# Performance work log

Measured on AMD Instinct MI355X. Metric: run time of the kernel, lower is better.

Reference implementation:

```python
import jax, jax.numpy as jnp
import numpy as np


def setup_inputs() -> dict:
    key = jax.random.key(0)
    k1, k2, k3, k4 = jax.random.split(key, 4)
    n, m = 4096, 1024  # n video frames, 1024-d features
    scale = 0.02
    return {
        "x": jax.random.normal(k1, (n, m), dtype=jnp.float32),
        "WQ": jax.random.normal(k2, (m, m), dtype=jnp.float32) * scale,  # torch Linear weight [out,in]
        "WK": jax.random.normal(k3, (m, m), dtype=jnp.float32) * scale,
        "WV": jax.random.normal(k4, (m, m), dtype=jnp.float32) * scale,
    }


def _quaternion_logits(q, k):
    """Hamilton-product attention logits: 4 tensors of shape [Lq, Lk]."""
    qr, qx, qy, qz = jnp.split(q, 4, axis=-1)
    kr, kx, ky, kz = jnp.split(k, 4, axis=-1)
    dot = lambda a, b: jnp.einsum('qd,kd->qk', a, b)
    r = dot(qr, kr) - dot(qx, kx) - dot(qy, ky) - dot(qz, kz)
    i = dot(qr, kx) + dot(qx, kr) + dot(qy, kz) - dot(qz, ky)
    j = dot(qr, ky) - dot(qx, kz) + dot(qy, kr) + dot(qz, kx)
    kk = dot(qr, kz) + dot(qx, ky) - dot(qy, kx) + dot(qz, kr)
    return [r, i, j, kk]


def reference(x, WQ, WK, WV):
    # QKV projections (torch Linear, no bias): y = x @ W.T
    Q = x @ WQ.T
    K = x @ WK.T
    V = x @ WV.T
    v_vals = jnp.split(V, 4, axis=-1)  # 4 chunks of depth d/4 (tensor2tensor quaternion attn)
    logits = _quaternion_logits(Q, K)
    outs = []
    w = None
    for l, v in zip(logits, v_vals):
        w = jax.nn.softmax(l, axis=-1)  # per-component softmax over keys
        outs.append(w @ v)
    y = jnp.concatenate(outs, axis=-1)  # [n, d]
    # original returns the attention weights from the last component (loop-leaked var)
    return y, w
```

## Files before the change

kernel.cpp:

```cpp
#include <hip/hip_runtime.h>
#include <cmath>

typedef __attribute__((ext_vector_type(8))) short short8;
typedef __attribute__((ext_vector_type(8))) _Float16 half8;
typedef __attribute__((ext_vector_type(4))) float f32x4;
typedef unsigned short u16;

__device__ __forceinline__ u16 f2h(float f) {
    _Float16 h = (_Float16)f;
    return __builtin_bit_cast(u16, h);
}
__device__ __forceinline__ float h2f(u16 b) {
    return (float)__builtin_bit_cast(_Float16, b);
}

#define GLD16(g, l)                                                              \
    __builtin_amdgcn_global_load_lds(                                            \
        (const __attribute__((address_space(1))) unsigned int*)(g),              \
        (__attribute__((address_space(3))) unsigned int*)(l), 16, 0, 0)

#define MFMA_F16(a, b, c)                                                        \
    __builtin_amdgcn_mfma_f32_16x16x32_f16(                                      \
        __builtin_bit_cast(half8, (a)), __builtin_bit_cast(half8, (b)), (c), 0, 0, 0)
#define SBAR() asm volatile("s_barrier" ::: "memory")

__global__ __launch_bounds__(256) void to_h(const float* __restrict__ in,
                                            u16* __restrict__ out) {
    int idx = blockIdx.x * 256 + threadIdx.x;
    float4 v = reinterpret_cast<const float4*>(in)[idx];
    ushort4 h;
    h.x = f2h(v.x); h.y = f2h(v.y); h.z = f2h(v.z); h.w = f2h(v.w);
    reinterpret_cast<ushort4*>(out)[idx] = h;
}

__global__ __launch_bounds__(512, 2) void logits8(
    const u16* __restrict__ A, const u16* __restrict__ B, const u16* __restrict__ Bneg,
    u16* __restrict__ Ch, float* __restrict__ pm, float* __restrict__ ps,
    int perm_packed, int sign_packed)
{
    constexpr int NT = 16;
    __shared__ u16 L[2][2][256 * 64];
    const int tid = threadIdx.x;
    const int l = tid & 63, w = tid >> 6;
    const int wr = w >> 2, wc = w & 3;
    const int lr = l & 15, lh = l >> 4;
    const int bid = (int)blockIdx.x;
    const int swz = (bid & 7) * 32 + (bid >> 3);
    const int row0 = (swz >> 4) * 256, col0 = (swz & 15) * 256;
    const int srow = l >> 3;
    const int scol = ((l & 7) ^ (l >> 3)) * 8;

    f32x4 acc[8][4] = {};

    auto stage = [&](int t) {
        int kA = t * 64;
        int ch = kA >> 8;
        int p = (perm_packed >> (2 * ch)) & 3;
        const u16* Bsrc = ((sign_packed >> ch) & 1) ? Bneg : B;
        int kB = (p << 8) + (kA & 255);
        int bf = t & 1;
        #pragma unroll
        for (int i = 0; i < 4; ++i) {
            int r0 = w * 32 + i * 8;
            GLD16(&A[(size_t)(row0 + r0 + srow) * 1024 + kA + scol], &L[bf][0][r0 * 64]);
        }
        #pragma unroll
        for (int i = 0; i < 4; ++i) {
            int r0 = w * 32 + i * 8;
            GLD16(&Bsrc[(size_t)(col0 + r0 + srow) * 1024 + kB + scol], &L[bf][1][r0 * 64]);
        }
    };
    auto readA = [&](int bf, int m, int kh) -> short8 {
        int row = wr * 128 + m * 16 + lr;
        int c = ((kh * 4 + lh) ^ (lr & 7)) * 8;
        return *reinterpret_cast<const short8*>(&L[bf][0][row * 64 + c]);
    };
    auto readB = [&](int bf, int n, int kh) -> short8 {
        int row = wc * 64 + n * 16 + lr;
        int c = ((kh * 4 + lh) ^ (lr & 7)) * 8;
        return *reinterpret_cast<const short8*>(&L[bf][1][row * 64 + c]);
    };

    stage(0);
    stage(1);
    asm volatile("s_waitcnt vmcnt(8)" ::: "memory");
    SBAR();

    #pragma unroll 2
    for (int t = 0; t < NT; ++t) {
        const int bf = t & 1;
        short8 am[4][2], bn[4][2];
        #pragma unroll
        for (int m = 0; m < 4; ++m) { am[m][0] = readA(bf, m, 0); am[m][1] = readA(bf, m, 1); }
        #pragma unroll
        for (int n = 0; n < 2; ++n) { bn[n][0] = readB(bf, n, 0); bn[n][1] = readB(bf, n, 1); }
        SBAR();
        __builtin_amdgcn_s_setprio(1);
        #pragma unroll
        for (int m = 0; m < 4; ++m)
            #pragma unroll
            for (int n = 0; n < 2; ++n) {
                acc[m][n] = MFMA_F16(am[m][0], bn[n][0], acc[m][n]);
                acc[m][n] = MFMA_F16(am[m][1], bn[n][1], acc[m][n]);
            }
        __builtin_amdgcn_s_setprio(0);
        SBAR();
        #pragma unroll
        for (int n = 2; n < 4; ++n) { bn[n][0] = readB(bf, n, 0); bn[n][1] = readB(bf, n, 1); }
        SBAR();
        __builtin_amdgcn_s_setprio(1);
        #pragma unroll
        for (int m = 0; m < 4; ++m)
            #pragma unroll
            for (int n = 2; n < 4; ++n) {
                acc[m][n] = MFMA_F16(am[m][0], bn[n][0], acc[m][n]);
                acc[m][n] = MFMA_F16(am[m][1], bn[n][1], acc[m][n]);
            }
        __builtin_amdgcn_s_setprio(0);
        SBAR();
        #pragma unroll
        for (int m = 0; m < 4; ++m) { am[m][0] = readA(bf, 4 + m, 0); am[m][1] = readA(bf, 4 + m, 1); }
        SBAR();
        __builtin_amdgcn_s_setprio(1);
        #pragma unroll
        for (int m = 0; m < 4; ++m)
            #pragma unroll
            for (int n = 2; n < 4; ++n) {
                acc[4 + m][n] = MFMA_F16(am[m][0], bn[n][0], acc[4 + m][n]);
                acc[4 + m][n] = MFMA_F16(am[m][1], bn[n][1], acc[4 + m][n]);
            }
        __builtin_amdgcn_s_setprio(0);
        SBAR();
        if (t + 2 < NT) stage(t + 2);
        SBAR();
        __builtin_amdgcn_s_setprio(1);
        #pragma unroll
        for (int m = 0; m < 4; ++m)
            #pragma unroll
            for (int n = 0; n < 2; ++n) {
                acc[4 + m][n] = MFMA_F16(am[m][0], bn[n][0], acc[4 + m][n]);
                acc[4 + m][n] = MFMA_F16(am[m][1], bn[n][1], acc[4 + m][n]);
            }
        __builtin_amdgcn_s_setprio(0);
        if (t + 2 < NT) { asm volatile("s_waitcnt vmcnt(8)" ::: "memory"); }
        else           { asm volatile("s_waitcnt vmcnt(0)" ::: "memory"); }
        SBAR();
    }

    const int tcol = (col0 >> 6) + wc;
    #pragma unroll
    for (int m = 0; m < 8; ++m) {
        #pragma unroll
        for (int j = 0; j < 4; ++j) {
            int row = row0 + wr * 128 + m * 16 + lh * 4 + j;
            float v = fmaxf(fmaxf(acc[m][0][j], acc[m][1][j]),
                            fmaxf(acc[m][2][j], acc[m][3][j]));
            #pragma unroll
            for (int off = 1; off < 16; off <<= 1) v = fmaxf(v, __shfl_xor(v, off, 16));
            float s = expf(acc[m][0][j] - v) + expf(acc[m][1][j] - v)
                    + expf(acc[m][2][j] - v) + expf(acc[m][3][j] - v);
            #pragma unroll
            for (int off = 1; off < 16; off <<= 1) s += __shfl_xor(s, off, 16);
            if (lr == 0) {
                pm[(size_t)row * 64 + tcol] = v;
                ps[(size_t)row * 64 + tcol] = s;
            }
            #pragma unroll
            for (int n = 0; n < 4; ++n) {
                int gc = col0 + wc * 64 + n * 16 + lr;
                Ch[(size_t)row * 4096 + gc] = f2h(acc[m][n][j] - v);
            }
        }
    }
}

__global__ __launch_bounds__(512, 2) void qkv8(
    const u16* __restrict__ A, const u16* __restrict__ B,
    u16* __restrict__ Qh, u16* __restrict__ Kh, u16* __restrict__ Khn,
    u16* __restrict__ Vt)
{
    constexpr int NT = 16;
    __shared__ u16 L[2][2][256 * 64];
    const int tid = threadIdx.x;
    const int l = tid & 63, w = tid >> 6;
    const int wr = w >> 2, wc = w & 3;
    const int lr = l & 15, lh = l >> 4;
    const int bid = (int)blockIdx.x;
    const int wgid = (bid & 7) * 24 + (bid >> 3);
    const int row0 = (wgid / 12) * 256, col0 = (wgid % 12) * 256;
    const int srow = l >> 3;
    const int scol = ((l & 7) ^ (l >> 3)) * 8;

    f32x4 acc[8][4] = {};

    auto stage = [&](int t) {
        int k0 = t * 64;
        int bf = t & 1;
        #pragma unroll
        for (int i = 0; i < 4; ++i) {
            int r0 = w * 32 + i * 8;
            GLD16(&A[(size_t)(row0 + r0 + srow) * 1024 + k0 + scol], &L[bf][0][r0 * 64]);
        }
        #pragma unroll
        for (int i = 0; i < 4; ++i) {
            int r0 = w * 32 + i * 8;
            GLD16(&B[(size_t)(col0 + r0 + srow) * 1024 + k0 + scol], &L[bf][1][r0 * 64]);
        }
    };
    auto readA = [&](int bf, int m, int kh) -> short8 {
        int row = wr * 128 + m * 16 + lr;
        int c = ((kh * 4 + lh) ^ (lr & 7)) * 8;
        return *reinterpret_cast<const short8*>(&L[bf][0][row * 64 + c]);
    };
    auto readB = [&](int bf, int n, int kh) -> short8 {
        int row = wc * 64 + n * 16 + lr;
        int c = ((kh * 4 + lh) ^ (lr & 7)) * 8;
        return *reinterpret_cast<const short8*>(&L[bf][1][row * 64 + c]);
    };

    stage(0);
    stage(1);
    asm volatile("s_waitcnt vmcnt(8)" ::: "memory");
    SBAR();

    #pragma unroll 2
    for (int t = 0; t < NT; ++t) {
        const int bf = t & 1;
        short8 am[4][2], bn[4][2];
        #pragma unroll
        for (int m = 0; m < 4; ++m) { am[m][0] = readA(bf, m, 0); am[m][1] = readA(bf, m, 1); }
        #pragma unroll
        for (int n = 0; n < 2; ++n) { bn[n][0] = readB(bf, n, 0); bn[n][1] = readB(bf, n, 1); }
        SBAR();
        __builtin_amdgcn_s_setprio(1);
        #pragma unroll
        for (int m = 0; m < 4; ++m)
            #pragma unroll
            for (int n = 0; n < 2; ++n) {
                acc[m][n] = MFMA_F16(am[m][0], bn[n][0], acc[m][n]);
                acc[m][n] = MFMA_F16(am[m][1], bn[n][1], acc[m][n]);
            }
        __builtin_amdgcn_s_setprio(0);
        SBAR();
        #pragma unroll
        for (int n = 2; n < 4; ++n) { bn[n][0] = readB(bf, n, 0); bn[n][1] = readB(bf, n, 1); }
        SBAR();
        __builtin_amdgcn_s_setprio(1);
        #pragma unroll
        for (int m = 0; m < 4; ++m)
            #pragma unroll
            for (int n = 2; n < 4; ++n) {
                acc[m][n] = MFMA_F16(am[m][0], bn[n][0], acc[m][n]);
                acc[m][n] = MFMA_F16(am[m][1], bn[n][1], acc[m][n]);
            }
        __builtin_amdgcn_s_setprio(0);
        SBAR();
        #pragma unroll
        for (int m = 0; m < 4; ++m) { am[m][0] = readA(bf, 4 + m, 0); am[m][1] = readA(bf, 4 + m, 1); }
        SBAR();
        __builtin_amdgcn_s_setprio(1);
        #pragma unroll
        for (int m = 0; m < 4; ++m)
            #pragma unroll
            for (int n = 2; n < 4; ++n) {
                acc[4 + m][n] = MFMA_F16(am[m][0], bn[n][0], acc[4 + m][n]);
                acc[4 + m][n] = MFMA_F16(am[m][1], bn[n][1], acc[4 + m][n]);
            }
        __builtin_amdgcn_s_setprio(0);
        SBAR();
        if (t + 2 < NT) stage(t + 2);
        SBAR();
        __builtin_amdgcn_s_setprio(1);
        #pragma unroll
        for (int m = 0; m < 4; ++m)
            #pragma unroll
            for (int n = 0; n < 2; ++n) {
                acc[4 + m][n] = MFMA_F16(am[m][0], bn[n][0], acc[4 + m][n]);
                acc[4 + m][n] = MFMA_F16(am[m][1], bn[n][1], acc[4 + m][n]);
            }
        __builtin_amdgcn_s_setprio(0);
        if (t + 2 < NT) { asm volatile("s_waitcnt vmcnt(8)" ::: "memory"); }
        else           { asm volatile("s_waitcnt vmcnt(0)" ::: "memory"); }
        SBAR();
    }

    const int mode = col0 >> 10;
    #pragma unroll
    for (int m = 0; m < 8; ++m)
        #pragma unroll
        for (int n = 0; n < 4; ++n) {
            int gr = row0 + wr * 128 + m * 16 + lh * 4;
            int gc = col0 + wc * 64 + n * 16 + lr;
            int gcl = gc & 1023;
            f32x4 v = acc[m][n];
            if (mode == 0) {
                #pragma unroll
                for (int j = 0; j < 4; ++j)
                    Qh[(size_t)(gr + j) * 1024 + gcl] = f2h(v[j]);
            } else if (mode == 1) {
                #pragma unroll
                for (int j = 0; j < 4; ++j) {
                    u16 h = f2h(v[j]);
                    size_t o = (size_t)(gr + j) * 1024 + gcl;
                    Kh[o] = h; Khn[o] = h ^ 0x8000;
                }
            } else {
                ushort4 o;
                o.x = f2h(v[0]); o.y = f2h(v[1]); o.z = f2h(v[2]); o.w = f2h(v[3]);
                *reinterpret_cast<ushort4*>(&Vt[(size_t)gcl * 4096 + gr]) = o;
            }
        }
}

template<bool WRITE_W>
__global__ __launch_bounds__(256) void pv_fused(
    const u16* __restrict__ Lh, float* __restrict__ Wout,
    const u16* __restrict__ Vt, const float* __restrict__ pm,
    const float* __restrict__ ps, u16* __restrict__ ypart, int c256)
{
    __shared__ u16 As[64 * 64];
    __shared__ u16 Bs[256 * 64];
    __shared__ float Red[64][4];
    __shared__ float Ms[64], Is[64];
    const int tid = threadIdx.x;
    const int l = tid & 63, w = tid >> 6;
    const int lr = l & 15, lh = l >> 4;
    const int kc = blockIdx.x;
    const int row0 = blockIdx.y * 64;
    const int kbase = kc * 512;
    const int srow = l >> 3, scol = ((l & 7) ^ (l >> 3)) * 8;

    {
        int row = tid & 63, part = tid >> 6;
        const float* pmr = &pm[(size_t)(row0 + row) * 64 + part * 16];
        const float* psr = &ps[(size_t)(row0 + row) * 64 + part * 16];
        float M = -INFINITY;
        #pragma unroll
        for (int i = 0; i < 16; ++i) M = fmaxf(M, pmr[i]);
        Red[row][part] = M;
        __syncthreads();
        float Mg = fmaxf(fmaxf(Red[row][0], Red[row][1]),
                         fmaxf(Red[row][2], Red[row][3]));
        float S = 0.f;
        #pragma unroll
        for (int i = 0; i < 16; ++i) S += psr[i] * expf(pmr[i] - Mg);
        __syncthreads();
        Red[row][part] = S;
        __syncthreads();
        if (tid < 64) {
            float Sg = Red[tid][0] + Red[tid][1] + Red[tid][2] + Red[tid][3];
            Ms[tid] = Mg;
            Is[tid] = 1.0f / Sg;
        }
        __syncthreads();
    }

    float Mr[4], Ir[4];
    #pragma unroll
    for (int i = 0; i < 4; ++i) { int r = (tid >> 4) + i * 16; Mr[i] = Ms[r]; Ir[i] = Is[r]; }

    f32x4 acc[4][4] = {};

    for (int kt = 0; kt < 8; ++kt) {
        const int tcol = kc * 8 + kt;
        __syncthreads();
        #pragma unroll
        for (int i = 0; i < 4; ++i) {
            int idx = tid + i * 256;
            int r = idx >> 4, s4 = idx & 15;
            float coff = pm[(size_t)(row0 + r) * 64 + tcol] - Mr[i];
            size_t ga = (size_t)(row0 + r) * 4096 + kbase + kt * 64 + s4 * 4;
            ushort4 dv = *reinterpret_cast<const ushort4*>(&Lh[ga]);
            float e0 = expf(h2f(dv.x) + coff) * Ir[i];
            float e1 = expf(h2f(dv.y) + coff) * Ir[i];
            float e2 = expf(h2f(dv.z) + coff) * Ir[i];
            float e3 = expf(h2f(dv.w) + coff) * Ir[i];
            if (WRITE_W)
                *reinterpret_cast<float4*>(&Wout[ga]) = make_float4(e0, e1, e2, e3);
            ushort4 h;
            h.x = f2h(e0); h.y = f2h(e1); h.z = f2h(e2); h.w = f2h(e3);
            int dst = ((s4 >> 1) ^ (r & 7)) * 8 + (s4 & 1) * 4;
            *reinterpret_cast<ushort4*>(&As[r * 64 + dst]) = h;
        }
        #pragma unroll
        for (int i = 0; i < 8; ++i) {
            int r0 = w * 64 + i * 8;
            GLD16(&Vt[(size_t)(c256 + r0 + srow) * 4096 + kbase + kt * 64 + scol],
                  &Bs[r0 * 64]);
        }
        __syncthreads();
        #pragma unroll
        for (int kh = 0; kh < 2; ++kh) {
            short8 af[4], bfv[4];
            #pragma unroll
            for (int m = 0; m < 4; ++m)
                af[m] = *reinterpret_cast<const short8*>(
                    &As[(m * 16 + lr) * 64 + ((kh * 4 + lh) ^ (lr & 7)) * 8]);
            #pragma unroll
            for (int n = 0; n < 4; ++n)
                bfv[n] = *reinterpret_cast<const short8*>(
                    &Bs[(w * 64 + n * 16 + lr) * 64 + ((kh * 4 + lh) ^ (lr & 7)) * 8]);
            #pragma unroll
            for (int m = 0; m < 4; ++m)
                #pragma unroll
                for (int n = 0; n < 4; ++n)
                    acc[m][n] = MFMA_F16(af[m], bfv[n], acc[m][n]);
        }
    }

    #pragma unroll
    for (int m = 0; m < 4; ++m)
        #pragma unroll
        for (int n = 0; n < 4; ++n) {
            int rr = m * 16 + lh * 4;
            int col = w * 64 + n * 16 + lr;
            #pragma unroll
            for (int j = 0; j < 4; ++j)
                ypart[((size_t)kc * 4096 + row0 + rr + j) * 256 + col] = f2h(acc[m][n][j]);
        }
}

__global__ __launch_bounds__(256) void reduce_y(const u16* __restrict__ ypart,
                                                float* __restrict__ y, int c256)
{
    int idx = blockIdx.x * 256 + threadIdx.x;
    int r = idx >> 6, c4 = (idx & 63) * 4;
    float s0 = 0.f, s1 = 0.f, s2 = 0.f, s3 = 0.f;
    #pragma unroll
    for (int kc = 0; kc < 8; ++kc) {
        ushort4 p = *reinterpret_cast<const ushort4*>(
            &ypart[((size_t)kc * 4096 + r) * 256 + c4]);
        s0 += h2f(p.x); s1 += h2f(p.y); s2 += h2f(p.z); s3 += h2f(p.w);
    }
    *reinterpret_cast<float4*>(&y[(size_t)r * 1024 + c256 + c4]) =
        make_float4(s0, s1, s2, s3);
}

extern "C" void kernel_launch(void* const* d_in, const int* in_sizes, int n_in,
                              void* d_out, int out_size, void* d_ws, size_t ws_size,
                              hipStream_t stream)
{
    const int n = 4096, d = 1024;
    const float* x  = (const float*)d_in[0];
    const float* WQ = (const float*)d_in[1];
    const float* WK = (const float*)d_in[2];
    const float* WV = (const float*)d_in[3];

    float* y = (float*)d_out;
    float* wout = y + (size_t)n * d;

    u16* Lh   = (u16*)d_ws;
    u16* xh   = Lh;
    u16* Wh   = Lh + (size_t)n * 1024;
    u16* Qh   = Lh + (size_t)n * 4096;
    u16* Kh   = Qh  + (size_t)n * 1024;
    u16* Khn  = Kh  + (size_t)n * 1024;
    u16* Vt   = Khn + (size_t)n * 1024;
    u16* ypart = Vt + (size_t)d * 4096;
    float* pm = (float*)(ypart + (size_t)8 * n * 256);
    float* ps = pm + (size_t)n * 64;

    to_h<<<n * d / 1024, 256, 0, stream>>>(x, xh);
    to_h<<<d * d / 1024, 256, 0, stream>>>(WQ, Wh);
    to_h<<<d * d / 1024, 256, 0, stream>>>(WK, Wh + (size_t)d * 1024);
    to_h<<<d * d / 1024, 256, 0, stream>>>(WV, Wh + (size_t)2 * d * 1024);

    qkv8<<<192, 512, 0, stream>>>(xh, Wh, Qh, Kh, Khn, Vt);

    const int permv[4] = {0xE4, 0xB1, 0x4E, 0x1B};
    const int signv[4] = {0x0E, 0x08, 0x02, 0x04};

    for (int c = 0; c < 4; ++c) {
        logits8<<<256, 512, 0, stream>>>(Qh, Kh, Khn, Lh, pm, ps, permv[c], signv[c]);
        if (c == 3)
            pv_fused<true><<<dim3(8, 64), 256, 0, stream>>>(Lh, wout, Vt, pm, ps, ypart, c * 256);
        else
            pv_fused<false><<<dim3(8, 64), 256, 0, stream>>>(Lh, wout, Vt, pm, ps, ypart, c * 256);
        reduce_y<<<1024, 256, 0, stream>>>(ypart, y, c * 256);
    }
}
```

Before: 374.3 us.

## Fuse conversions, negate A in registers, store exp in logits, atomic-add partial outputs

Folds the four fp16 conversion launches into one kernel. Drops the negated-K copy and instead flips sign bits on the A fragments in registers. The logits kernel now stores exp(l - local max) instead of raw offsets, so the PV kernel applies one per-tile scale rather than an exp per element, and it loads 8-wide vectors. The partial-sum buffer and the reduce_y launches are replaced by float atomicAdd into a zeroed y. This removes launches and global traffic, at the cost of atomic contention, a nondeterministic summation order, and fp16 underflow risk for the stored exponentials.

```diff
diff --git a/kernel.cpp b/kernel.cpp
--- a/kernel.cpp
+++ b/kernel.cpp
@@ -2,8 +2,10 @@
 #include <cmath>
 
 typedef __attribute__((ext_vector_type(8))) short short8;
+typedef __attribute__((ext_vector_type(8))) unsigned short ushort8_t;
 typedef __attribute__((ext_vector_type(8))) _Float16 half8;
 typedef __attribute__((ext_vector_type(4))) float f32x4;
+typedef __attribute__((ext_vector_type(4))) unsigned int u32x4;
 typedef unsigned short u16;
 
 __device__ __forceinline__ u16 f2h(float f) {
@@ -12,6 +14,11 @@
 }
 __device__ __forceinline__ float h2f(u16 b) {
     return (float)__builtin_bit_cast(_Float16, b);
+}
+__device__ __forceinline__ short8 neg16(short8 v) {
+    u32x4 u = __builtin_bit_cast(u32x4, v);
+    u ^= 0x80008000u;
+    return __builtin_bit_cast(short8, u);
 }
 
 #define GLD16(g, l)                                                              \
@@ -24,18 +31,33 @@
         __builtin_bit_cast(half8, (a)), __builtin_bit_cast(half8, (b)), (c), 0, 0, 0)
 #define SBAR() asm volatile("s_barrier" ::: "memory")
 
-__global__ __launch_bounds__(256) void to_h(const float* __restrict__ in,
-                                            u16* __restrict__ out) {
-    int idx = blockIdx.x * 256 + threadIdx.x;
-    float4 v = reinterpret_cast<const float4*>(in)[idx];
+__global__ __launch_bounds__(256) void to_h_all(
+    const float* __restrict__ x, const float* __restrict__ WQ,
+    const float* __restrict__ WK, const float* __restrict__ WV,
+    u16* __restrict__ xh, u16* __restrict__ Wh)
+{
+    int bid = blockIdx.x;
+    const float* src;
+    u16* dst;
+    int off;
+    if (bid < 4096) { src = x; dst = xh; off = bid; }
+    else {
+        int j = bid - 4096;
+        int wsel = j >> 10;
+        off = j & 1023;
+        src = wsel == 0 ? WQ : (wsel == 1 ? WK : WV);
+        dst = Wh + (size_t)wsel * 1024 * 1024;
+    }
+    int idx = off * 256 + threadIdx.x;
+    float4 v = reinterpret_cast<const float4*>(src)[idx];
     ushort4 h;
     h.x = f2h(v.x); h.y = f2h(v.y); h.z = f2h(v.z); h.w = f2h(v.w);
-    reinterpret_cast<ushort4*>(out)[idx] = h;
+    reinterpret_cast<ushort4*>(dst)[idx] = h;
 }
 
 __global__ __launch_bounds__(512, 2) void logits8(
-    const u16* __restrict__ A, const u16* __restrict__ B, const u16* __restrict__ Bneg,
-    u16* __restrict__ Ch, float* __restrict__ pm, float* __restrict__ ps,
+    const u16* __restrict__ A, const u16* __restrict__ B,
+    u16* __restrict__ P, float* __restrict__ pm, float* __restrict__ ps,
     int perm_packed, int sign_packed)
 {
     constexpr int NT = 16;
@@ -56,7 +78,6 @@
         int kA = t * 64;
         int ch = kA >> 8;
         int p = (perm_packed >> (2 * ch)) & 3;
-        const u16* Bsrc = ((sign_packed >> ch) & 1) ? Bneg : B;
         int kB = (p << 8) + (kA & 255);
         int bf = t & 1;
         #pragma unroll
@@ -67,7 +88,7 @@
         #pragma unroll
         for (int i = 0; i < 4; ++i) {
             int r0 = w * 32 + i * 8;
-            GLD16(&Bsrc[(size_t)(col0 + r0 + srow) * 1024 + kB + scol], &L[bf][1][r0 * 64]);
+            GLD16(&B[(size_t)(col0 + r0 + srow) * 1024 + kB + scol], &L[bf][1][r0 * 64]);
         }
     };
     auto readA = [&](int bf, int m, int kh) -> short8 {
@@ -89,9 +110,13 @@
     #pragma unroll 2
     for (int t = 0; t < NT; ++t) {
         const int bf = t & 1;
+        const bool sgn = (sign_packed >> (t >> 2)) & 1;
         short8 am[4][2], bn[4][2];
         #pragma unroll
         for (int m = 0; m < 4; ++m) { am[m][0] = readA(bf, m, 0); am[m][1] = readA(bf, m, 1); }
+        if (sgn)
+            #pragma unroll
+            for (int m = 0; m < 4; ++m) { am[m][0] = neg16(am[m][0]); am[m][1] = neg16(am[m][1]); }
         #pragma unroll
         for (int n = 0; n < 2; ++n) { bn[n][0] = readB(bf, n, 0); bn[n][1] = readB(bf, n, 1); }
         SBAR();
@@ -120,6 +145,9 @@
         SBAR();
         #pragma unroll
         for (int m = 0; m < 4; ++m) { am[m][0] = readA(bf, 4 + m, 0); am[m][1] = readA(bf, 4 + m, 1); }
+        if (sgn)
+            #pragma unroll
+            for (int m = 0; m < 4; ++m) { am[m][0] = neg16(am[m][0]); am[m][1] = neg16(am[m][1]); }
         SBAR();
         __builtin_amdgcn_s_setprio(1);
         #pragma unroll
@@ -157,8 +185,10 @@
                             fmaxf(acc[m][2][j], acc[m][3][j]));
             #pragma unroll
             for (int off = 1; off < 16; off <<= 1) v = fmaxf(v, __shfl_xor(v, off, 16));
-            float s = expf(acc[m][0][j] - v) + expf(acc[m][1][j] - v)
-                    + expf(acc[m][2][j] - v) + expf(acc[m][3][j] - v);
+            float e[4];
+            #pragma unroll
+            for (int n = 0; n < 4; ++n) e[n] = expf(acc[m][n][j] - v);
+            float s = e[0] + e[1] + e[2] + e[3];
             #pragma unroll
             for (int off = 1; off < 16; off <<= 1) s += __shfl_xor(s, off, 16);
             if (lr == 0) {
@@ -168,7 +198,7 @@
             #pragma unroll
             for (int n = 0; n < 4; ++n) {
                 int gc = col0 + wc * 64 + n * 16 + lr;
-                Ch[(size_t)row * 4096 + gc] = f2h(acc[m][n][j] - v);
+                P[(size_t)row * 4096 + gc] = f2h(e[n]);
             }
         }
     }
@@ -176,8 +206,7 @@
 
 __global__ __launch_bounds__(512, 2) void qkv8(
     const u16* __restrict__ A, const u16* __restrict__ B,
-    u16* __restrict__ Qh, u16* __restrict__ Kh, u16* __restrict__ Khn,
-    u16* __restrict__ Vt)
+    u16* __restrict__ Qh, u16* __restrict__ Kh, u16* __restrict__ Vt)
 {
     constexpr int NT = 16;
     __shared__ u16 L[2][2][256 * 64];
@@ -299,11 +328,8 @@
                     Qh[(size_t)(gr + j) * 1024 + gcl] = f2h(v[j]);
             } else if (mode == 1) {
                 #pragma unroll
-                for (int j = 0; j < 4; ++j) {
-                    u16 h = f2h(v[j]);
-                    size_t o = (size_t)(gr + j) * 1024 + gcl;
-                    Kh[o] = h; Khn[o] = h ^ 0x8000;
-                }
+                for (int j = 0; j < 4; ++j)
+                    Kh[(size_t)(gr + j) * 1024 + gcl] = f2h(v[j]);
             } else {
                 ushort4 o;
                 o.x = f2h(v[0]); o.y = f2h(v[1]); o.z = f2h(v[2]); o.w = f2h(v[3]);
@@ -314,9 +340,9 @@
 
 template<bool WRITE_W>
 __global__ __launch_bounds__(256) void pv_fused(
-    const u16* __restrict__ Lh, float* __restrict__ Wout,
+    const u16* __restrict__ P, float* __restrict__ Wout,
     const u16* __restrict__ Vt, const float* __restrict__ pm,
-    const float* __restrict__ ps, u16* __restrict__ ypart, int c256)
+    const float* __restrict__ ps, float* __restrict__ Y, int c256)
 {
     __shared__ u16 As[64 * 64];
     __shared__ u16 Bs[256 * 64];
@@ -355,9 +381,9 @@
         __syncthreads();
     }
 
-    float Mr[4], Ir[4];
-    #pragma unroll
-    for (int i = 0; i < 4; ++i) { int r = (tid >> 4) + i * 16; Mr[i] = Ms[r]; Ir[i] = Is[r]; }
+    const int r0 = tid >> 3;
+    const float M0 = Ms[r0], I0 = Is[r0];
+    const float M1 = Ms[r0 + 32], I1 = Is[r0 + 32];
 
     f32x4 acc[4][4] = {};
 
@@ -365,28 +391,33 @@
         const int tcol = kc * 8 + kt;
         __syncthreads();
         #pragma unroll
-        for (int i = 0; i < 4; ++i) {
-            int idx = tid + i * 256;
-            int r = idx >> 4, s4 = idx & 15;
-            float coff = pm[(size_t)(row0 + r) * 64 + tcol] - Mr[i];
-            size_t ga = (size_t)(row0 + r) * 4096 + kbase + kt * 64 + s4 * 4;
-            ushort4 dv = *reinterpret_cast<const ushort4*>(&Lh[ga]);
-            float e0 = expf(h2f(dv.x) + coff) * Ir[i];
-            float e1 = expf(h2f(dv.y) + coff) * Ir[i];
-            float e2 = expf(h2f(dv.z) + coff) * Ir[i];
-            float e3 = expf(h2f(dv.w) + coff) * Ir[i];
-            if (WRITE_W)
-                *reinterpret_cast<float4*>(&Wout[ga]) = make_float4(e0, e1, e2, e3);
-            ushort4 h;
-            h.x = f2h(e0); h.y = f2h(e1); h.z = f2h(e2); h.w = f2h(e3);
-            int dst = ((s4 >> 1) ^ (r & 7)) * 8 + (s4 & 1) * 4;
-            *reinterpret_cast<ushort4*>(&As[r * 64 + dst]) = h;
+        for (int i = 0; i < 2; ++i) {
+            int r = r0 + i * 32;
+            int s8 = tid & 7;
+            float Mv = i ? M1 : M0, Iv = i ? I1 : I0;
+            float alpha = expf(pm[(size_t)(row0 + r) * 64 + tcol] - Mv) * Iv;
+            size_t ga = (size_t)(row0 + r) * 4096 + kbase + kt * 64 + s8 * 8;
+            ushort8_t p8 = *reinterpret_cast<const ushort8_t*>(&P[ga]);
+            ushort8_t w8;
+            float wf[8];
+            #pragma unroll
+            for (int e = 0; e < 8; ++e) {
+                wf[e] = h2f(p8[e]) * alpha;
+                w8[e] = f2h(wf[e]);
+            }
+            if (WRITE_W) {
+                *reinterpret_cast<float4*>(&Wout[ga]) =
+                    make_float4(wf[0], wf[1], wf[2], wf[3]);
+                *reinterpret_cast<float4*>(&Wout[ga + 4]) =
+                    make_float4(wf[4], wf[5], wf[6], wf[7]);
+            }
+            *reinterpret_cast<ushort8_t*>(&As[r * 64 + (s8 ^ (r & 7)) * 8]) = w8;
         }
         #pragma unroll
         for (int i = 0; i < 8; ++i) {
-            int r0 = w * 64 + i * 8;
-            GLD16(&Vt[(size_t)(c256 + r0 + srow) * 4096 + kbase + kt * 64 + scol],
-                  &Bs[r0 * 64]);
+            int rb = w * 64 + i * 8;
+            GLD16(&Vt[(size_t)(c256 + rb + srow) * 4096 + kbase + kt * 64 + scol],
+                  &Bs[rb * 64]);
         }
         __syncthreads();
         #pragma unroll
@@ -413,27 +444,11 @@
         #pragma unroll
         for (int n = 0; n < 4; ++n) {
             int rr = m * 16 + lh * 4;
-            int col = w * 64 + n * 16 + lr;
+            int col = c256 + w * 64 + n * 16 + lr;
             #pragma unroll
             for (int j = 0; j < 4; ++j)
-                ypart[((size_t)kc * 4096 + row0 + rr + j) * 256 + col] = f2h(acc[m][n][j]);
-        }
-}
-
-__global__ __launch_bounds__(256) void reduce_y(const u16* __restrict__ ypart,
-                                                float* __restrict__ y, int c256)
-{
-    int idx = blockIdx.x * 256 + threadIdx.x;
-    int r = idx >> 6, c4 = (idx & 63) * 4;
-    float s0 = 0.f, s1 = 0.f, s2 = 0.f, s3 = 0.f;
-    #pragma unroll
-    for (int kc = 0; kc < 8; ++kc) {
-        ushort4 p = *reinterpret_cast<const ushort4*>(
-            &ypart[((size_t)kc * 4096 + r) * 256 + c4]);
-        s0 += h2f(p.x); s1 += h2f(p.y); s2 += h2f(p.z); s3 += h2f(p.w);
-    }
-    *reinterpret_cast<float4*>(&y[(size_t)r * 1024 + c256 + c4]) =
-        make_float4(s0, s1, s2, s3);
+                atomicAdd(&Y[(size_t)(row0 + rr + j) * 1024 + col], acc[m][n][j]);
+        }
 }
 
 extern "C" void kernel_launch(void* const* d_in, const int* in_sizes, int n_in,
@@ -449,33 +464,29 @@
     float* y = (float*)d_out;
     float* wout = y + (size_t)n * d;
 
-    u16* Lh   = (u16*)d_ws;
-    u16* xh   = Lh;
-    u16* Wh   = Lh + (size_t)n * 1024;
-    u16* Qh   = Lh + (size_t)n * 4096;
-    u16* Kh   = Qh  + (size_t)n * 1024;
-    u16* Khn  = Kh  + (size_t)n * 1024;
-    u16* Vt   = Khn + (size_t)n * 1024;
-    u16* ypart = Vt + (size_t)d * 4096;
-    float* pm = (float*)(ypart + (size_t)8 * n * 256);
+    u16* P    = (u16*)d_ws;
+    u16* xh   = P;
+    u16* Wh   = P + (size_t)n * 1024;
+    u16* Qh   = P + (size_t)n * 4096;
+    u16* Kh   = Qh + (size_t)n * 1024;
+    u16* Vt   = Kh + (size_t)n * 1024;
+    float* pm = (float*)(Vt + (size_t)d * 4096);
     float* ps = pm + (size_t)n * 64;
 
-    to_h<<<n * d / 1024, 256, 0, stream>>>(x, xh);
-    to_h<<<d * d / 1024, 256, 0, stream>>>(WQ, Wh);
-    to_h<<<d * d / 1024, 256, 0, stream>>>(WK, Wh + (size_t)d * 1024);
-    to_h<<<d * d / 1024, 256, 0, stream>>>(WV, Wh + (size_t)2 * d * 1024);
-
-    qkv8<<<192, 512, 0, stream>>>(xh, Wh, Qh, Kh, Khn, Vt);
+    hipMemsetAsync(y, 0, (size_t)n * d * sizeof(float), stream);
+
+    to_h_all<<<7168, 256, 0, stream>>>(x, WQ, WK, WV, xh, Wh);
+
+    qkv8<<<192, 512, 0, stream>>>(xh, Wh, Qh, Kh, Vt);
 
     const int permv[4] = {0xE4, 0xB1, 0x4E, 0x1B};
     const int signv[4] = {0x0E, 0x08, 0x02, 0x04};
 
     for (int c = 0; c < 4; ++c) {
-        logits8<<<256, 512, 0, stream>>>(Qh, Kh, Khn, Lh, pm, ps, permv[c], signv[c]);
+        logits8<<<256, 512, 0, stream>>>(Qh, Kh, P, pm, ps, permv[c], signv[c]);
         if (c == 3)
-            pv_fused<true><<<dim3(8, 64), 256, 0, stream>>>(Lh, wout, Vt, pm, ps, ypart, c * 256);
+            pv_fused<true><<<dim3(8, 64), 256, 0, stream>>>(P, wout, Vt, pm, ps, y, c * 256);
         else
-            pv_fused<false><<<dim3(8, 64), 256, 0, stream>>>(Lh, wout, Vt, pm, ps, ypart, c * 256);
-        reduce_y<<<1024, 256, 0, stream>>>(ypart, y, c * 256);
-    }
-}
+            pv_fused<false><<<dim3(8, 64), 256, 0, stream>>>(P, wout, Vt, pm, ps, y, c * 256);
+    }
+}
```

Result: slower. 507.2 us (+35.5%).
